# Kernel tuning notes

Measured on AMD Instinct MI355X. Metric: run time of the kernel, lower is better.

Reference implementation:

```python
import jax, jax.numpy as jnp
import numpy as np

B, N, M, K = 8, 9225, 4096, 32
D = 2          # coordinate dim
HID = 64       # MLP hidden
DOUT = 16      # MLP output / f_y channels


def setup_inputs() -> dict:
    key = jax.random.key(0)
    ks = jax.random.split(key, 10)
    y = jax.random.uniform(ks[0], (B, N, D), dtype=jnp.float32)
    x = jax.random.uniform(ks[1], (B, M, D), dtype=jnp.float32)
    f_y = jax.random.uniform(ks[2], (B, N, DOUT), dtype=jnp.float32)
    weights = jax.random.uniform(ks[3], (B, N), dtype=jnp.float32)
    neighbors_index = jax.random.randint(ks[4], (B, M, K), 0, N, dtype=jnp.int64)
    drop = jax.random.uniform(ks[5], (B, M, K)) < 0.1
    neighbors_index = jnp.where(drop, jnp.int64(-1), neighbors_index)
    # LinearChannelMLP params: 4 -> 64 -> 16, gelu between
    W1 = jax.random.normal(ks[6], (2 * D, HID), dtype=jnp.float32) * (1.0 / np.sqrt(2 * D))
    b1 = jnp.zeros((HID,), dtype=jnp.float32)
    W2 = jax.random.normal(ks[7], (HID, DOUT), dtype=jnp.float32) * (1.0 / np.sqrt(HID))
    b2 = jnp.zeros((DOUT,), dtype=jnp.float32)
    return {"y": y, "x": x, "f_y": f_y, "weights": weights,
            "W1": W1, "b1": b1, "W2": W2, "b2": b2,
            "neighbors_index": neighbors_index}


def _batched_gather(table, idx):
    # table: [B, N, ...], idx: [B, M, K] -> [B, M, K, ...]
    return jax.vmap(lambda t, i: t[i])(table, idx)


def reference(y, x, f_y, weights, W1, b1, W2, b2, neighbors_index):
    idx = jnp.where(neighbors_index == -1, 0, neighbors_index)      # [B,M,K]
    valid = (neighbors_index != -1).astype(y.dtype)[..., None]      # [B,M,K,1]

    rep_y = _batched_gather(y, idx)                                 # [B,M,K,D]
    in_f = _batched_gather(f_y, idx)                                # [B,M,K,DOUT]
    self_x = jnp.broadcast_to(x[:, :, None, :], rep_y.shape)        # [B,M,K,D]

    agg = jnp.concatenate([rep_y, self_x], axis=-1)                 # [B,M,K,2D]
    h = jax.nn.gelu(agg @ W1 + b1, approximate=False)               # [B,M,K,HID]
    kval = h @ W2 + b2                                              # [B,M,K,DOUT]

    kval = kval * in_f                                              # linear transform: k(x,y)*f(y)
    w_nbr = _batched_gather(weights, idx)[..., None]                # [B,M,K,1]
    kval = kval * w_nbr * valid
    return kval.sum(axis=2)                                         # [B,M,DOUT]
```

## Files before the change

kernel.cpp:

```cpp
#include <hip/hip_runtime.h>
#include <hip/hip_bf16.h>

#define B_    8
#define N_    9225
#define M_    4096
#define K_    32
#define HID_  64
#define DOUT_ 16

typedef __attribute__((ext_vector_type(8))) short short8;
typedef __attribute__((ext_vector_type(4))) float floatx4;
typedef __attribute__((ext_vector_type(2))) float f32x2;

static __device__ __forceinline__ short f2bf(float f) {
    __hip_bfloat16 h = __float2bfloat16(f);
    return __builtin_bit_cast(short, h);
}
static __device__ __forceinline__ f32x2 splat2(float v) { return (f32x2){v, v}; }
static __device__ __forceinline__ int bpermi(int src_bytes, int v) {
    return __builtin_amdgcn_ds_bpermute(src_bytes, v);
}
static __device__ __forceinline__ float bpermf(int src_bytes, float v) {
    return __builtin_bit_cast(float,
        __builtin_amdgcn_ds_bpermute(src_bytes, __builtin_bit_cast(int, v)));
}

static __device__ __forceinline__ float row16_sum(float v) {
    int t;
    t = __builtin_amdgcn_update_dpp(0, __builtin_bit_cast(int, v), 0x111, 0xF, 0xF, true);
    v += __builtin_bit_cast(float, t);
    t = __builtin_amdgcn_update_dpp(0, __builtin_bit_cast(int, v), 0x112, 0xF, 0xF, true);
    v += __builtin_bit_cast(float, t);
    t = __builtin_amdgcn_update_dpp(0, __builtin_bit_cast(int, v), 0x114, 0xF, 0xF, true);
    v += __builtin_bit_cast(float, t);
    t = __builtin_amdgcn_update_dpp(0, __builtin_bit_cast(int, v), 0x118, 0xF, 0xF, true);
    v += __builtin_bit_cast(float, t);
    return v;
}

static __device__ __forceinline__ f32x2 gelu2(f32x2 x) {
    const f32x2 xsq = x * x;
    const f32x2 t   = __builtin_elementwise_fma(xsq, splat2(0.035677408f), splat2(0.79788456f));
    const f32x2 z   = x * t;
    const f32x2 u   = z * z;
    const f32x2 a   = u + splat2(105.0f);
    const f32x2 nin = __builtin_elementwise_fma(u, a, splat2(945.0f));
    const f32x2 num = z * nin;
    const f32x2 bq  = __builtin_elementwise_fma(u, splat2(15.0f), splat2(420.0f));
    const f32x2 den = __builtin_elementwise_fma(u, bq, splat2(945.0f));
    const f32x2 r   = { __builtin_amdgcn_rcpf(den[0]), __builtin_amdgcn_rcpf(den[1]) };
    f32x2 th = num * r;
    th = __builtin_elementwise_min(__builtin_elementwise_max(th, splat2(-1.0f)), splat2(1.0f));
    const f32x2 hx = x * splat2(0.5f);
    return __builtin_elementwise_fma(hx, th, hx);
}

__global__ __launch_bounds__(256) void it_kernel(
    const float* __restrict__ y,
    const float* __restrict__ x,
    const float* __restrict__ f_y,
    const float* __restrict__ weights,
    const float* __restrict__ W1,
    const float* __restrict__ b1,
    const float* __restrict__ W2,
    const float* __restrict__ b2,
    const int*   __restrict__ nbr,
    float*       __restrict__ out)
{
    __shared__ float W1L[4][64];
    __shared__ float b1L[64];
    __shared__ float b2L[16];

    const int tid  = threadIdx.x;
    W1L[tid >> 6][tid & 63] = W1[tid];
    if (tid < 64) b1L[tid] = b1[tid];
    if (tid < 16) b2L[tid] = b2[tid];

    const int lane = tid & 63;
    const int q    = lane >> 4;
    const int nlo  = lane & 15;
    const int row0 = __builtin_amdgcn_readfirstlane((blockIdx.x * 4 + (tid >> 6)) * 2);
    const int bbase = (row0 >> 12) * N_;

    const int r_g = lane >> 5, kk = lane & 31;
    const int raw = nbr[(size_t)(row0 + r_g) * K_ + kk];
    const int vld = raw >= 0;
    const int bn_g = bbase + (vld ? raw : 0);
    const float2 yvg = *(const float2*)(y + (size_t)bn_g * 2);
    const float  wg  = vld ? weights[bn_g] : 0.0f;

    short8 w2f[2];
    #pragma unroll
    for (int ch = 0; ch < 2; ++ch)
        #pragma unroll
        for (int jj = 0; jj < 8; ++jj)
            w2f[ch][jj] = f2bf(W2[(ch*32 + q*8 + jj) * DOUT_ + nlo]);

    __syncthreads();

    float partial[4] = {0.f, 0.f, 0.f, 0.f};
    #pragma unroll
    for (int ph = 0; ph < 4; ++ph) {
        const int it = ph >> 1, h = ph & 1;
        const int src = ((it << 5) + (h << 4) + nlo) << 2;

        const int bn = bpermi(src, bn_g);
        const floatx4 fv = *(const floatx4*)(f_y + (size_t)bn * 16 + q * 4);

        f32x2 yv;
        yv[0] = bpermf(src, yvg.x);
        yv[1] = bpermf(src, yvg.y);
        const float s = bpermf(src, wg);
        const float2 xv = *(const float2*)(x + (size_t)(row0 + it) * 2);

        short8 hf[2];
        #pragma unroll
        for (int ch = 0; ch < 2; ++ch) {
            #pragma unroll
            for (int p = 0; p < 4; ++p) {
                const int j = ch*32 + q*8 + 2*p;
                f32x2 hin = *(const f32x2*)&b1L[j];
                hin = __builtin_elementwise_fma(splat2(yv[0]), *(const f32x2*)&W1L[0][j], hin);
                hin = __builtin_elementwise_fma(splat2(yv[1]), *(const f32x2*)&W1L[1][j], hin);
                hin = __builtin_elementwise_fma(splat2(xv.x),  *(const f32x2*)&W1L[2][j], hin);
                hin = __builtin_elementwise_fma(splat2(xv.y),  *(const f32x2*)&W1L[3][j], hin);
                const f32x2 g = gelu2(hin);
                hf[ch][2*p]     = f2bf(g[0]);
                hf[ch][2*p + 1] = f2bf(g[1]);
            }
        }
        floatx4 acc = *(const floatx4*)&b2L[q*4];
        acc = __builtin_amdgcn_mfma_f32_16x16x32_bf16(w2f[0], hf[0], acc, 0, 0, 0);
        acc = __builtin_amdgcn_mfma_f32_16x16x32_bf16(w2f[1], hf[1], acc, 0, 0, 0);
        #pragma unroll
        for (int r4 = 0; r4 < 4; ++r4)
            partial[r4] = fmaf(acc[r4], fv[r4] * s, partial[r4]);

        if (h == 1) {
            #pragma unroll
            for (int r4 = 0; r4 < 4; ++r4)
                partial[r4] = row16_sum(partial[r4]);
            if (nlo == 15) {
                floatx4 o = {partial[0], partial[1], partial[2], partial[3]};
                *(floatx4*)(out + (size_t)(row0 + it) * DOUT_ + q*4) = o;
            }
            #pragma unroll
            for (int r4 = 0; r4 < 4; ++r4) partial[r4] = 0.f;
        }
    }
}

extern "C" void kernel_launch(void* const* d_in, const int* in_sizes, int n_in,
                              void* d_out, int out_size, void* d_ws, size_t ws_size,
                              hipStream_t stream) {
    const float* y   = (const float*)d_in[0];
    const float* x   = (const float*)d_in[1];
    const float* f_y = (const float*)d_in[2];
    const float* w   = (const float*)d_in[3];
    const float* W1  = (const float*)d_in[4];
    const float* b1  = (const float*)d_in[5];
    const float* W2  = (const float*)d_in[6];
    const float* b2  = (const float*)d_in[7];
    const int*   nbr = (const int*)d_in[8];
    float* out = (float*)d_out;

    dim3 grid(B_ * M_ / 8), block(256);
    hipLaunchKernelGGL(it_kernel, grid, block, 0, stream,
                       y, x, f_y, w, W1, b1, W2, b2, nbr, out);
}
```

Measured before the change: 109.2 us.

## Make waves persistent over four row pairs with software-prefetched neighbor gathers

```diff
diff --git a/kernel.cpp b/kernel.cpp
--- a/kernel.cpp
+++ b/kernel.cpp
@@ -7,6 +7,8 @@
 #define K_    32
 #define HID_  64
 #define DOUT_ 16
+#define NWAVES 4096
+#define ITERS  4
 
 typedef __attribute__((ext_vector_type(8))) short short8;
 typedef __attribute__((ext_vector_type(4))) float floatx4;
@@ -79,15 +81,8 @@
     const int lane = tid & 63;
     const int q    = lane >> 4;
     const int nlo  = lane & 15;
-    const int row0 = __builtin_amdgcn_readfirstlane((blockIdx.x * 4 + (tid >> 6)) * 2);
-    const int bbase = (row0 >> 12) * N_;
-
-    const int r_g = lane >> 5, kk = lane & 31;
-    const int raw = nbr[(size_t)(row0 + r_g) * K_ + kk];
-    const int vld = raw >= 0;
-    const int bn_g = bbase + (vld ? raw : 0);
-    const float2 yvg = *(const float2*)(y + (size_t)bn_g * 2);
-    const float  wg  = vld ? weights[bn_g] : 0.0f;
+    const int r_g  = lane >> 5, kk = lane & 31;
+    const int wid  = __builtin_amdgcn_readfirstlane(blockIdx.x * 4 + (tid >> 6));
 
     short8 w2f[2];
     #pragma unroll
@@ -96,57 +91,91 @@
         for (int jj = 0; jj < 8; ++jj)
             w2f[ch][jj] = f2bf(W2[(ch*32 + q*8 + jj) * DOUT_ + nlo]);
 
+    int row0 = wid * 2;
+    {
+    }
+    int raw = nbr[(size_t)(row0 + r_g) * K_ + kk];
+    float2 xv0 = *(const float2*)(x + (size_t)row0 * 2);
+    float2 xv1 = *(const float2*)(x + (size_t)row0 * 2 + 2);
+    int   vld  = raw >= 0;
+    int   bn_g = (row0 >> 12) * N_ + (vld ? raw : 0);
+    float2 yvg = *(const float2*)(y + (size_t)bn_g * 2);
+    float  wg  = vld ? weights[bn_g] : 0.0f;
+
     __syncthreads();
 
-    float partial[4] = {0.f, 0.f, 0.f, 0.f};
-    #pragma unroll
-    for (int ph = 0; ph < 4; ++ph) {
-        const int it = ph >> 1, h = ph & 1;
-        const int src = ((it << 5) + (h << 4) + nlo) << 2;
+    for (int itn = 0; itn < ITERS; ++itn) {
+        const int row0n = row0 + NWAVES * 2;
 
-        const int bn = bpermi(src, bn_g);
-        const floatx4 fv = *(const floatx4*)(f_y + (size_t)bn * 16 + q * 4);
+        int raw_n = 0; float2 xv0_n = {0,0}, xv1_n = {0,0};
+        if (itn + 1 < ITERS) {
+            raw_n  = nbr[(size_t)(row0n + r_g) * K_ + kk];
+            xv0_n  = *(const float2*)(x + (size_t)row0n * 2);
+            xv1_n  = *(const float2*)(x + (size_t)row0n * 2 + 2);
+        }
+        int bn_gn = 0; float2 yvg_n = {0,0}; float wg_n = 0.0f;
 
-        f32x2 yv;
-        yv[0] = bpermf(src, yvg.x);
-        yv[1] = bpermf(src, yvg.y);
-        const float s = bpermf(src, wg);
-        const float2 xv = *(const float2*)(x + (size_t)(row0 + it) * 2);
+        float partial[4] = {0.f, 0.f, 0.f, 0.f};
+        #pragma unroll
+        for (int ph = 0; ph < 4; ++ph) {
+            const int it = ph >> 1, h = ph & 1;
+            const int src = ((it << 5) + (h << 4) + nlo) << 2;
 
-        short8 hf[2];
-        #pragma unroll
-        for (int ch = 0; ch < 2; ++ch) {
+            const int bn = bpermi(src, bn_g);
+            const floatx4 fv = *(const floatx4*)(f_y + (size_t)bn * 16 + q * 4);
+
+            f32x2 yv;
+            yv[0] = bpermf(src, yvg.x);
+            yv[1] = bpermf(src, yvg.y);
+            const float s = bpermf(src, wg);
+            const float2 xv = it ? xv1 : xv0;
+
+            short8 hf[2];
             #pragma unroll
-            for (int p = 0; p < 4; ++p) {
-                const int j = ch*32 + q*8 + 2*p;
-                f32x2 hin = *(const f32x2*)&b1L[j];
-                hin = __builtin_elementwise_fma(splat2(yv[0]), *(const f32x2*)&W1L[0][j], hin);
-                hin = __builtin_elementwise_fma(splat2(yv[1]), *(const f32x2*)&W1L[1][j], hin);
-                hin = __builtin_elementwise_fma(splat2(xv.x),  *(const f32x2*)&W1L[2][j], hin);
-                hin = __builtin_elementwise_fma(splat2(xv.y),  *(const f32x2*)&W1L[3][j], hin);
-                const f32x2 g = gelu2(hin);
-                hf[ch][2*p]     = f2bf(g[0]);
-                hf[ch][2*p + 1] = f2bf(g[1]);
+            for (int ch = 0; ch < 2; ++ch) {
+                #pragma unroll
+                for (int p = 0; p < 4; ++p) {
+                    const int j = ch*32 + q*8 + 2*p;
+                    f32x2 hin = *(const f32x2*)&b1L[j];
+                    hin = __builtin_elementwise_fma(splat2(yv[0]), *(const f32x2*)&W1L[0][j], hin);
+                    hin = __builtin_elementwise_fma(splat2(yv[1]), *(const f32x2*)&W1L[1][j], hin);
+                    hin = __builtin_elementwise_fma(splat2(xv.x),  *(const f32x2*)&W1L[2][j], hin);
+                    hin = __builtin_elementwise_fma(splat2(xv.y),  *(const f32x2*)&W1L[3][j], hin);
+                    const f32x2 g = gelu2(hin);
+                    hf[ch][2*p]     = f2bf(g[0]);
+                    hf[ch][2*p + 1] = f2bf(g[1]);
+                }
+            }
+            floatx4 acc = *(const floatx4*)&b2L[q*4];
+            acc = __builtin_amdgcn_mfma_f32_16x16x32_bf16(w2f[0], hf[0], acc, 0, 0, 0);
+            acc = __builtin_amdgcn_mfma_f32_16x16x32_bf16(w2f[1], hf[1], acc, 0, 0, 0);
+            #pragma unroll
+            for (int r4 = 0; r4 < 4; ++r4)
+                partial[r4] = fmaf(acc[r4], fv[r4] * s, partial[r4]);
+
+            if (h == 1) {
+                #pragma unroll
+                for (int r4 = 0; r4 < 4; ++r4)
+                    partial[r4] = row16_sum(partial[r4]);
+                if (nlo == 15) {
+                    floatx4 o = {partial[0], partial[1], partial[2], partial[3]};
+                    *(floatx4*)(out + (size_t)(row0 + it) * DOUT_ + q*4) = o;
+                }
+                #pragma unroll
+                for (int r4 = 0; r4 < 4; ++r4) partial[r4] = 0.f;
+            }
+
+            if (ph == 1 && itn + 1 < ITERS) {
+                const int vld_n = raw_n >= 0;
+                bn_gn = (row0n >> 12) * N_ + (vld_n ? raw_n : 0);
+                yvg_n = *(const float2*)(y + (size_t)bn_gn * 2);
+                wg_n  = vld_n ? weights[bn_gn] : 0.0f;
             }
         }
-        floatx4 acc = *(const floatx4*)&b2L[q*4];
-        acc = __builtin_amdgcn_mfma_f32_16x16x32_bf16(w2f[0], hf[0], acc, 0, 0, 0);
-        acc = __builtin_amdgcn_mfma_f32_16x16x32_bf16(w2f[1], hf[1], acc, 0, 0, 0);
-        #pragma unroll
-        for (int r4 = 0; r4 < 4; ++r4)
-            partial[r4] = fmaf(acc[r4], fv[r4] * s, partial[r4]);
 
-        if (h == 1) {
-            #pragma unroll
-            for (int r4 = 0; r4 < 4; ++r4)
-                partial[r4] = row16_sum(partial[r4]);
-            if (nlo == 15) {
-                floatx4 o = {partial[0], partial[1], partial[2], partial[3]};
-                *(floatx4*)(out + (size_t)(row0 + it) * DOUT_ + q*4) = o;
-            }
-            #pragma unroll
-            for (int r4 = 0; r4 < 4; ++r4) partial[r4] = 0.f;
-        }
+        row0 = row0n;
+        bn_g = bn_gn; yvg = yvg_n; wg = wg_n;
+        xv0 = xv0_n; xv1 = xv1_n;
     }
 }
 
@@ -164,7 +193,7 @@
     const int*   nbr = (const int*)d_in[8];
     float* out = (float*)d_out;
 
-    dim3 grid(B_ * M_ / 8), block(256);
+    dim3 grid(NWAVES / 4), block(256);
     hipLaunchKernelGGL(it_kernel, grid, block, 0, stream,
                        y, x, f_y, w, W1, b1, W2, b2, nbr, out);
 }
```

Result: no change. 107.3 us (-1.7%).
